# Optimization experiments

Hardware: AMD Instinct MI355X
Metric: run time of the kernel (lower is better)

The kernel has to match this reference:

```python
import jax, jax.numpy as jnp
import numpy as np

N_NODES = 100000
N_EDGES = 1600000
D_IN = 50
HIDDEN = 128
N_CLASSES = 8


def setup_inputs() -> dict:
    key = jax.random.key(0)
    ks = jax.random.split(key, 8)
    x = jax.random.normal(ks[0], (N_NODES, D_IN), dtype=jnp.float32)
    edge_index = jax.random.randint(ks[1], (2, N_EDGES), 0, N_NODES, dtype=jnp.int64)
    s1 = 1.0 / np.sqrt(D_IN)
    s2 = 1.0 / np.sqrt(HIDDEN)
    return {
        "x": x,
        "edge_index": edge_index,
        "W1_l": jax.random.normal(ks[2], (D_IN, HIDDEN), dtype=jnp.float32) * s1,
        "W1_r": jax.random.normal(ks[3], (D_IN, HIDDEN), dtype=jnp.float32) * s1,
        "b1": jnp.zeros((HIDDEN,), dtype=jnp.float32),
        "W2_l": jax.random.normal(ks[4], (HIDDEN, N_CLASSES), dtype=jnp.float32) * s2,
        "W2_r": jax.random.normal(ks[5], (HIDDEN, N_CLASSES), dtype=jnp.float32) * s2,
        "b2": jnp.zeros((N_CLASSES,), dtype=jnp.float32),
    }


def _sage_conv(h, src, dst, n_nodes, W_l, W_r, b):
    # mean aggregation of neighbor messages src -> dst
    msg = h[src]                                                   # [E, d]
    agg = jax.ops.segment_sum(msg, dst, num_segments=n_nodes)      # [N, d]
    deg = jax.ops.segment_sum(jnp.ones((src.shape[0], 1), h.dtype), dst,
                              num_segments=n_nodes)                # [N, 1]
    agg = agg / jnp.maximum(deg, 1.0)
    # PyG SAGEConv: lin_l(aggregated) + lin_r(root), bias in lin_l
    return agg @ W_l + h @ W_r + b


def reference(x, edge_index, W1_l, W1_r, b1, W2_l, W2_r, b2):
    n_nodes = x.shape[0]
    src, dst = edge_index[0], edge_index[1]
    h = jax.nn.relu(_sage_conv(x, src, dst, n_nodes, W1_l, W1_r, b1))
    # dropout p=0.5 is identity in eval mode (deterministic baseline)
    return _sage_conv(h, src, dst, n_nodes, W2_l, W2_r, b2)
```

## Files before the change

### kernel.cpp

```cpp
#include <hip/hip_runtime.h>

#define N_NODES 100000
#define N_EDGES 1600000
#define D_IN    50
#define HIDDEN  128
#define NCLS    8

#define TILE    4096
#define NTILES  ((N_EDGES + TILE - 1) / TILE)
#define BSHIFT  9
#define NB      196

#define PREP_CONVX_BLOCKS 12500
#define PREP_W_BLOCKS     36

#define LW 68

typedef __bf16 bf16_t;
typedef bf16_t bf16x8 __attribute__((ext_vector_type(8)));
typedef float  f32x4  __attribute__((ext_vector_type(4)));

__device__ __forceinline__ unsigned f2bf(float f) {
    union { float f; unsigned u; } a; a.f = f;
    unsigned u = a.u;
    return (u + 0x7FFFu + ((u >> 16) & 1u)) >> 16;
}
__device__ __forceinline__ unsigned pack2(float a, float b) {
    return f2bf(a) | (f2bf(b) << 16);
}
__device__ __forceinline__ float bf_lo(unsigned v) { return __uint_as_float(v << 16); }
__device__ __forceinline__ float bf_hi(unsigned v) { return __uint_as_float(v & 0xFFFF0000u); }

__global__ __launch_bounds__(256) void prep_kernel(
    const float* __restrict__ x,
    const int*   __restrict__ dst,
    const float* __restrict__ W1l, const float* __restrict__ W1r,
    const float* __restrict__ W2l, const float* __restrict__ W2r,
    unsigned* __restrict__ xb, unsigned* __restrict__ acat,
    int* __restrict__ g_hist, int* __restrict__ btot,
    unsigned* __restrict__ Wt1g, unsigned* __restrict__ W2tg)
{
    __shared__ int lh[NB];
    int blk = blockIdx.x;
    int tid = threadIdx.x;

    if (blk < PREP_CONVX_BLOCKS) {
        int t = blk * 256 + tid;
        int n = t >> 5, j = t & 31;
        if (j < 25) {
            float2 v = ((const float2*)x)[n * 25 + j];
            unsigned pk = pack2(v.x, v.y);
            xb[n * 25 + j] = pk;
            acat[(size_t)n * 64 + 25 + j] = pk;
        } else {
            int z = n * 64 + 50 + (j - 25) * 2;
            acat[z] = 0u;
            acat[z + 1] = 0u;
        }
    } else if (blk < PREP_CONVX_BLOCKS + NTILES) {
        int tile = blk - PREP_CONVX_BLOCKS;
        for (int i = tid; i < NB; i += 256) lh[i] = 0;
        __syncthreads();
        int base = tile * TILE;
        int cnt = min(TILE, N_EDGES - base);
        for (int i = tid; i < cnt; i += 256)
            atomicAdd(&lh[dst[base + i] >> BSHIFT], 1);
        __syncthreads();
        for (int i = tid; i < NB; i += 256) {
            int v = lh[i];
            g_hist[tile * NB + i] = v;
            if (v) atomicAdd(&btot[i], v);
        }
    } else {
        int t = (blk - PREP_CONVX_BLOCKS - NTILES) * 256 + tid;
        if (t < 8192) {
            int n = t >> 6, kp = t & 63;
            int k0 = kp * 2, k1 = k0 + 1;
            float v0 = (k0 < 50) ? W1l[k0 * 128 + n] : ((k0 < 100) ? W1r[(k0 - 50) * 128 + n] : 0.0f);
            float v1 = (k1 < 50) ? W1l[k1 * 128 + n] : ((k1 < 100) ? W1r[(k1 - 50) * 128 + n] : 0.0f);
            Wt1g[t] = pack2(v0, v1);
        } else if (t < 8192 + 1024) {
            int u = t - 8192;
            int n2 = u >> 6, kp = u & 63;
            int k0 = kp * 2;
            float v0 = (n2 < 8) ? W2l[k0 * 8 + n2] : W2r[k0 * 8 + n2 - 8];
            float v1 = (n2 < 8) ? W2l[(k0 + 1) * 8 + n2] : W2r[(k0 + 1) * 8 + n2 - 8];
            W2tg[u] = pack2(v0, v1);
        }
    }
}

__global__ __launch_bounds__(512) void passB_kernel(
    int* __restrict__ g_hist, const int* __restrict__ btot,
    int* __restrict__ bbase, int* __restrict__ offs)
{
    __shared__ int s[512];
    int b = blockIdx.x, tid = threadIdx.x;
    int v = (tid < NTILES) ? g_hist[tid * NB + b] : 0;
    s[tid] = v;
    __syncthreads();
    for (int d = 1; d < 512; d <<= 1) {
        int t = (tid >= d) ? s[tid - d] : 0;
        __syncthreads();
        s[tid] += t;
        __syncthreads();
    }
    if (tid < NTILES) g_hist[tid * NB + b] = s[tid] - v;
    __syncthreads();

    int v2 = (tid < NB) ? btot[tid] : 0;
    s[tid] = v2;
    __syncthreads();
    for (int d = 1; d < 256; d <<= 1) {
        int t = (tid >= d && tid < 256) ? s[tid - d] : 0;
        __syncthreads();
        if (tid < 256) s[tid] += t;
        __syncthreads();
    }
    if (tid == b) bbase[b] = s[tid] - v2;
    if (b == 0 && tid == 0) offs[N_NODES] = N_EDGES;
}

__global__ __launch_bounds__(256) void passC_kernel(
    const int* __restrict__ src, const int* __restrict__ dst,
    const int* __restrict__ g_hist, const int* __restrict__ bbase,
    unsigned* __restrict__ bk_pack)
{
    __shared__ int hist[NB];
    __shared__ int seg[NB];
    __shared__ int cur[NB];
    __shared__ int gof[NB];
    __shared__ int sc[256];
    __shared__ unsigned s_pack[TILE];
    __shared__ unsigned short s_bkt[TILE];

    int tid = threadIdx.x, tile = blockIdx.x;
    int base = tile * TILE;
    int cnt = min(TILE, N_EDGES - base);

    for (int i = tid; i < NB; i += 256) {
        hist[i] = 0;
        gof[i] = g_hist[tile * NB + i] + bbase[i];
    }
    __syncthreads();

    int es[16], ed[16];
    #pragma unroll
    for (int k = 0; k < 16; ++k) {
        int i = tid + k * 256;
        if (i < cnt) {
            es[k] = src[base + i];
            ed[k] = dst[base + i];
            atomicAdd(&hist[ed[k] >> BSHIFT], 1);
        }
    }
    __syncthreads();

    {
        int v = (tid < NB) ? hist[tid] : 0;
        sc[tid] = v;
        __syncthreads();
        for (int d = 1; d < 256; d <<= 1) {
            int t = (tid >= d) ? sc[tid - d] : 0;
            __syncthreads();
            sc[tid] += t;
            __syncthreads();
        }
        if (tid < NB) { seg[tid] = sc[tid] - v; cur[tid] = sc[tid] - v; }
    }
    __syncthreads();

    #pragma unroll
    for (int k = 0; k < 16; ++k) {
        int i = tid + k * 256;
        if (i < cnt) {
            int b = ed[k] >> BSHIFT;
            int p = atomicAdd(&cur[b], 1);
            s_pack[p] = (unsigned)es[k] | ((unsigned)(ed[k] & 511) << 17);
            s_bkt[p] = (unsigned short)b;
        }
    }
    __syncthreads();

    for (int i = tid; i < cnt; i += 256) {
        int b = s_bkt[i];
        int g = gof[b] + (i - seg[b]);
        bk_pack[g] = s_pack[i];
    }
}

__global__ __launch_bounds__(512) void passD_kernel(
    const unsigned* __restrict__ bk_pack,
    const int* __restrict__ bbase, const int* __restrict__ btot,
    int* __restrict__ sorted_src, int* __restrict__ offs)
{
    __shared__ int ldeg[512];
    __shared__ int lofs[512];
    int b = blockIdx.x, tid = threadIdx.x;
    int ebase = bbase[b];
    int ecnt = btot[b];
    int nbase = b << BSHIFT;

    ldeg[tid] = 0;
    __syncthreads();
    for (int i = tid; i < ecnt; i += 512)
        atomicAdd(&ldeg[bk_pack[ebase + i] >> 17], 1);
    __syncthreads();

    int v = ldeg[tid];
    lofs[tid] = v;
    __syncthreads();
    for (int d = 1; d < 512; d <<= 1) {
        int t = (tid >= d) ? lofs[tid - d] : 0;
        __syncthreads();
        lofs[tid] += t;
        __syncthreads();
    }
    int ex = lofs[tid] - v;

    int node = nbase + tid;
    if (node < N_NODES) offs[node] = ebase + ex;

    ldeg[tid] = ex;
    __syncthreads();
    for (int i = tid; i < ecnt; i += 512) {
        unsigned pk = bk_pack[ebase + i];
        int p = atomicAdd(&ldeg[pk >> 17], 1);
        sorted_src[ebase + p] = (int)(pk & 0x1FFFFu);
    }
}

__global__ __launch_bounds__(256) void agg_x_kernel(
    const unsigned* __restrict__ xb,
    const int*      __restrict__ offs,
    const int*      __restrict__ ss,
    unsigned* __restrict__ acat)
{
    int node = blockIdx.x * 8 + (threadIdx.x >> 5);
    int dw   = threadIdx.x & 31;
    if (node >= N_NODES) return;
    int beg = offs[node], end = offs[node + 1];
    float2 a0 = {0.f,0.f}, a1 = {0.f,0.f}, a2 = {0.f,0.f}, a3 = {0.f,0.f};
    float2 a4 = {0.f,0.f}, a5 = {0.f,0.f}, a6 = {0.f,0.f}, a7 = {0.f,0.f};
    int i = beg;
    for (; i + 7 < end; i += 8) {
        int s0 = ss[i],     s1 = ss[i + 1], s2 = ss[i + 2], s3 = ss[i + 3];
        int s4 = ss[i + 4], s5 = ss[i + 5], s6 = ss[i + 6], s7 = ss[i + 7];
        if (dw < 25) {
            unsigned v0 = xb[s0 * 25 + dw];
            unsigned v1 = xb[s1 * 25 + dw];
            unsigned v2 = xb[s2 * 25 + dw];
            unsigned v3 = xb[s3 * 25 + dw];
            unsigned v4 = xb[s4 * 25 + dw];
            unsigned v5 = xb[s5 * 25 + dw];
            unsigned v6 = xb[s6 * 25 + dw];
            unsigned v7 = xb[s7 * 25 + dw];
            a0.x += bf_lo(v0); a0.y += bf_hi(v0);
            a1.x += bf_lo(v1); a1.y += bf_hi(v1);
            a2.x += bf_lo(v2); a2.y += bf_hi(v2);
            a3.x += bf_lo(v3); a3.y += bf_hi(v3);
            a4.x += bf_lo(v4); a4.y += bf_hi(v4);
            a5.x += bf_lo(v5); a5.y += bf_hi(v5);
            a6.x += bf_lo(v6); a6.y += bf_hi(v6);
            a7.x += bf_lo(v7); a7.y += bf_hi(v7);
        }
    }
    for (; i + 3 < end; i += 4) {
        int s0 = ss[i], s1 = ss[i + 1], s2 = ss[i + 2], s3 = ss[i + 3];
        if (dw < 25) {
            unsigned v0 = xb[s0 * 25 + dw];
            unsigned v1 = xb[s1 * 25 + dw];
            unsigned v2 = xb[s2 * 25 + dw];
            unsigned v3 = xb[s3 * 25 + dw];
            a0.x += bf_lo(v0); a0.y += bf_hi(v0);
            a1.x += bf_lo(v1); a1.y += bf_hi(v1);
            a2.x += bf_lo(v2); a2.y += bf_hi(v2);
            a3.x += bf_lo(v3); a3.y += bf_hi(v3);
        }
    }
    for (; i < end; ++i) {
        int s = ss[i];
        if (dw < 25) {
            unsigned v = xb[s * 25 + dw];
            a0.x += bf_lo(v); a0.y += bf_hi(v);
        }
    }
    if (dw < 25) {
        float inv = 1.0f / fmaxf((float)(end - beg), 1.0f);
        float sx = ((a0.x + a1.x) + (a2.x + a3.x)) + ((a4.x + a5.x) + (a6.x + a7.x));
        float sy = ((a0.y + a1.y) + (a2.y + a3.y)) + ((a4.y + a5.y) + (a6.y + a7.y));
        acat[(size_t)node * 64 + dw] = pack2(sx * inv, sy * inv);
    }
}

__global__ __launch_bounds__(256) void fused_mlp_kernel(
    const unsigned* __restrict__ Acat,
    const unsigned* __restrict__ Wt1g,
    const unsigned* __restrict__ W2tg,
    const float* __restrict__ b1,
    const float* __restrict__ b2,
    unsigned* __restrict__ pb,
    float* __restrict__ q)
{
    __shared__ unsigned sWt[128 * LW];
    __shared__ unsigned sW2t[16 * LW];
    __shared__ bf16_t   sH[4][16 * 136];

    int tid = threadIdx.x;
    for (int t = tid; t < 128 * 64; t += 256)
        sWt[(t >> 6) * LW + (t & 63)] = Wt1g[t];
    for (int t = tid; t < 16 * 64; t += 256)
        sW2t[(t >> 6) * LW + (t & 63)] = W2tg[t];
    __syncthreads();

    const int w    = tid >> 6;
    const int lane = tid & 63;
    const int lo   = lane & 15;
    const int g    = lane >> 4;

    float b1v[8][4];
    #pragma unroll
    for (int nt = 0; nt < 8; ++nt)
        #pragma unroll
        for (int r = 0; r < 4; ++r)
            b1v[nt][r] = b1[nt * 16 + g * 4 + r];
    float b2v[4];
    #pragma unroll
    for (int r = 0; r < 4; ++r)
        b2v[r] = (g >= 2) ? b2[(g - 2) * 4 + r] : 0.0f;

    bf16_t* myH = &sH[w][0];

    for (int tile = blockIdx.x; tile * 64 < N_NODES; tile += gridDim.x) {
        int node = tile * 64 + w * 16 + lo;
        int nclamp = min(node, N_NODES - 1);

        int4 bi[4];
        #pragma unroll
        for (int ks = 0; ks < 4; ++ks)
            bi[ks] = *((const int4*)(Acat + (size_t)nclamp * 64 + ks * 16 + g * 4));

        f32x4 acc[8];
        #pragma unroll
        for (int nt = 0; nt < 8; ++nt) acc[nt] = (f32x4)0.0f;
        #pragma unroll
        for (int nt = 0; nt < 8; ++nt) {
            #pragma unroll
            for (int ks = 0; ks < 4; ++ks) {
                int4 ai = *((const int4*)(sWt + (nt * 16 + lo) * LW + ks * 16 + g * 4));
                acc[nt] = __builtin_amdgcn_mfma_f32_16x16x32_bf16(
                    __builtin_bit_cast(bf16x8, ai),
                    __builtin_bit_cast(bf16x8, bi[ks]), acc[nt], 0, 0, 0);
            }
        }

        #pragma unroll
        for (int nt = 0; nt < 8; ++nt) {
            union { bf16_t h[4]; uint2 u; } pk;
            #pragma unroll
            for (int r = 0; r < 4; ++r)
                pk.h[r] = (bf16_t)fmaxf(acc[nt][r] + b1v[nt][r], 0.0f);
            *((uint2*)(myH + lo * 136 + nt * 16 + g * 4)) = pk.u;
        }
        __syncthreads();

        f32x4 acc2 = (f32x4)0.0f;
        #pragma unroll
        for (int ks = 0; ks < 4; ++ks) {
            int4 a2 = *((const int4*)(sW2t + lo * LW + ks * 16 + g * 4));
            int4 h2 = *((const int4*)(myH + lo * 136 + ks * 32 + g * 8));
            acc2 = __builtin_amdgcn_mfma_f32_16x16x32_bf16(
                __builtin_bit_cast(bf16x8, a2),
                __builtin_bit_cast(bf16x8, h2), acc2, 0, 0, 0);
        }

        if (node < N_NODES) {
            if (g < 2) {
                union { bf16_t h[4]; uint2 u; } pk;
                #pragma unroll
                for (int r = 0; r < 4; ++r) pk.h[r] = (bf16_t)acc2[r];
                *((uint2*)(pb + (size_t)node * 4 + g * 2)) = pk.u;
            } else {
                float4 qq;
                qq.x = acc2[0] + b2v[0];
                qq.y = acc2[1] + b2v[1];
                qq.z = acc2[2] + b2v[2];
                qq.w = acc2[3] + b2v[3];
                *((float4*)(q + (size_t)node * 8 + (g - 2) * 4)) = qq;
            }
        }
        __syncthreads();
    }
}

__global__ __launch_bounds__(256) void aggp_final_kernel(
    const unsigned* __restrict__ pb,
    const float*    __restrict__ q,
    const int*      __restrict__ offs,
    const int*      __restrict__ ss,
    float* __restrict__ out)
{
    int node = blockIdx.x * 4 + (threadIdx.x >> 6);
    int lane = threadIdx.x & 63;
    int k  = lane >> 2;
    int c2 = lane & 3;
    if (node >= N_NODES) return;
    int beg = offs[node], end = offs[node + 1];
    float2 acc = make_float2(0.0f, 0.0f);
    int i = beg + k;
    int sNext = (i < end) ? ss[i] : 0;
    for (; i < end; i += 16) {
        int s = sNext;
        int i2 = i + 16;
        sNext = (i2 < end) ? ss[i2] : 0;
        unsigned v = pb[s * 4 + c2];
        acc.x += bf_lo(v);
        acc.y += bf_hi(v);
    }
    acc.x += __shfl_xor(acc.x, 4);  acc.y += __shfl_xor(acc.y, 4);
    acc.x += __shfl_xor(acc.x, 8);  acc.y += __shfl_xor(acc.y, 8);
    acc.x += __shfl_xor(acc.x, 16); acc.y += __shfl_xor(acc.y, 16);
    acc.x += __shfl_xor(acc.x, 32); acc.y += __shfl_xor(acc.y, 32);
    if (lane < 4) {
        float inv = 1.0f / fmaxf((float)(end - beg), 1.0f);
        float2 qq = ((const float2*)(q + (size_t)node * NCLS))[c2];
        ((float2*)(out + (size_t)node * NCLS))[c2] =
            make_float2(acc.x * inv + qq.x, acc.y * inv + qq.y);
    }
}

extern "C" void kernel_launch(void* const* d_in, const int* in_sizes, int n_in,
                              void* d_out, int out_size, void* d_ws, size_t ws_size,
                              hipStream_t stream)
{
    const float* x   = (const float*)d_in[0];
    const int*   ei  = (const int*)  d_in[1];
    const float* W1l = (const float*)d_in[2];
    const float* W1r = (const float*)d_in[3];
    const float* b1  = (const float*)d_in[4];
    const float* W2l = (const float*)d_in[5];
    const float* W2r = (const float*)d_in[6];
    const float* b2  = (const float*)d_in[7];
    float* out = (float*)d_out;

    const int* src = ei;
    const int* dst = ei + N_EDGES;

    int* ws = (int*)d_ws;
    int*      offs       = ws;
    int*      g_hist     = offs + (N_NODES + 4);
    int*      btot       = g_hist + NTILES * NB;
    int*      bbase      = btot + 256;
    int*      sorted_src = bbase + 256;
    unsigned* xb         = (unsigned*)(sorted_src + N_EDGES);
    unsigned* Acat       = xb + (size_t)N_NODES * 25;
    unsigned* Wt1g       = Acat + (size_t)N_NODES * 64;
    unsigned* W2tg       = Wt1g + 8192;
    unsigned* pb         = W2tg + 1024;
    float*    q          = (float*)(pb + (size_t)N_NODES * 4);
    unsigned* bk_pack    = (unsigned*)(q + (size_t)N_NODES * 8);

    (void)hipMemsetAsync(btot, 0, NB * sizeof(int), stream);

    prep_kernel<<<PREP_CONVX_BLOCKS + NTILES + PREP_W_BLOCKS, 256, 0, stream>>>(
        x, dst, W1l, W1r, W2l, W2r, xb, Acat, g_hist, btot, Wt1g, W2tg);

    passB_kernel<<<NB, 512, 0, stream>>>(g_hist, btot, bbase, offs);
    passC_kernel<<<NTILES, 256, 0, stream>>>(src, dst, g_hist, bbase, bk_pack);
    passD_kernel<<<NB, 512, 0, stream>>>(bk_pack, bbase, btot, sorted_src, offs);

    agg_x_kernel<<<(N_NODES + 7) / 8, 256, 0, stream>>>(xb, offs, sorted_src, Acat);

    fused_mlp_kernel<<<512, 256, 0, stream>>>(Acat, Wt1g, W2tg, b1, b2, pb, q);

    aggp_final_kernel<<<(N_NODES + 3) / 4, 256, 0, stream>>>(
        (const unsigned*)pb, q, offs, sorted_src, out);
}
```

Baseline: 140.3 us.

## Pad bf16 features to 32 words and gather neighbours with 16-byte vector loads

The bf16 copy of x is padded from 25 to 32 words per row so that the first-layer neighbour gather can use uint4 loads. In each half-wave, four neighbours are processed in parallel with eight lanes per row, and the partial sums are combined with xor shuffles. This replaces 32-bit loads where 7 of 32 lanes sat idle. The sort tile is also halved to 2048 edges so more blocks run, and passB now scans two tiles per thread to handle the larger tile count. The cost is more memory for the padded array and some shuffle overhead.

```diff
diff --git a/kernel.cpp b/kernel.cpp
--- a/kernel.cpp
+++ b/kernel.cpp
@@ -6,7 +6,7 @@
 #define HIDDEN  128
 #define NCLS    8
 
-#define TILE    4096
+#define TILE    2048
 #define NTILES  ((N_EDGES + TILE - 1) / TILE)
 #define BSHIFT  9
 #define NB      196
@@ -30,6 +30,9 @@
 }
 __device__ __forceinline__ float bf_lo(unsigned v) { return __uint_as_float(v << 16); }
 __device__ __forceinline__ float bf_hi(unsigned v) { return __uint_as_float(v & 0xFFFF0000u); }
+
+#define ACC4(a, u) { a[0]+=bf_lo(u.x); a[1]+=bf_hi(u.x); a[2]+=bf_lo(u.y); a[3]+=bf_hi(u.y); \
+                     a[4]+=bf_lo(u.z); a[5]+=bf_hi(u.z); a[6]+=bf_lo(u.w); a[7]+=bf_hi(u.w); }
 
 __global__ __launch_bounds__(256) void prep_kernel(
     const float* __restrict__ x,
@@ -50,9 +53,10 @@
         if (j < 25) {
             float2 v = ((const float2*)x)[n * 25 + j];
             unsigned pk = pack2(v.x, v.y);
-            xb[n * 25 + j] = pk;
+            xb[n * 32 + j] = pk;
             acat[(size_t)n * 64 + 25 + j] = pk;
         } else {
+            xb[n * 32 + j] = 0u;
             int z = n * 64 + 50 + (j - 25) * 2;
             acat[z] = 0u;
             acat[z + 1] = 0u;
@@ -96,7 +100,10 @@
 {
     __shared__ int s[512];
     int b = blockIdx.x, tid = threadIdx.x;
-    int v = (tid < NTILES) ? g_hist[tid * NB + b] : 0;
+    int t0 = 2 * tid, t1 = 2 * tid + 1;
+    int v0 = (t0 < NTILES) ? g_hist[t0 * NB + b] : 0;
+    int v1 = (t1 < NTILES) ? g_hist[t1 * NB + b] : 0;
+    int v = v0 + v1;
     s[tid] = v;
     __syncthreads();
     for (int d = 1; d < 512; d <<= 1) {
@@ -105,16 +112,18 @@
         s[tid] += t;
         __syncthreads();
     }
-    if (tid < NTILES) g_hist[tid * NB + b] = s[tid] - v;
+    int ex = s[tid] - v;
+    if (t0 < NTILES) g_hist[t0 * NB + b] = ex;
+    if (t1 < NTILES) g_hist[t1 * NB + b] = ex + v0;
     __syncthreads();
 
     int v2 = (tid < NB) ? btot[tid] : 0;
     s[tid] = v2;
     __syncthreads();
-    for (int d = 1; d < 256; d <<= 1) {
-        int t = (tid >= d && tid < 256) ? s[tid - d] : 0;
-        __syncthreads();
-        if (tid < 256) s[tid] += t;
+    for (int d = 1; d < 512; d <<= 1) {
+        int t = (tid >= d) ? s[tid - d] : 0;
+        __syncthreads();
+        s[tid] += t;
         __syncthreads();
     }
     if (tid == b) bbase[b] = s[tid] - v2;
@@ -144,9 +153,9 @@
     }
     __syncthreads();
 
-    int es[16], ed[16];
+    int es[8], ed[8];
     #pragma unroll
-    for (int k = 0; k < 16; ++k) {
+    for (int k = 0; k < 8; ++k) {
         int i = tid + k * 256;
         if (i < cnt) {
             es[k] = src[base + i];
@@ -171,7 +180,7 @@
     __syncthreads();
 
     #pragma unroll
-    for (int k = 0; k < 16; ++k) {
+    for (int k = 0; k < 8; ++k) {
         int i = tid + k * 256;
         if (i < cnt) {
             int b = ed[k] >> BSHIFT;
@@ -231,65 +240,57 @@
 }
 
 __global__ __launch_bounds__(256) void agg_x_kernel(
-    const unsigned* __restrict__ xb,
-    const int*      __restrict__ offs,
-    const int*      __restrict__ ss,
+    const uint4* __restrict__ xb4,
+    const int*   __restrict__ offs,
+    const int*   __restrict__ ss,
     unsigned* __restrict__ acat)
 {
     int node = blockIdx.x * 8 + (threadIdx.x >> 5);
-    int dw   = threadIdx.x & 31;
+    int l32  = threadIdx.x & 31;
+    int slot = l32 >> 3;
+    int ld   = l32 & 7;
     if (node >= N_NODES) return;
     int beg = offs[node], end = offs[node + 1];
-    float2 a0 = {0.f,0.f}, a1 = {0.f,0.f}, a2 = {0.f,0.f}, a3 = {0.f,0.f};
-    float2 a4 = {0.f,0.f}, a5 = {0.f,0.f}, a6 = {0.f,0.f}, a7 = {0.f,0.f};
+    float a0[8] = {0,0,0,0,0,0,0,0};
+    float a1[8] = {0,0,0,0,0,0,0,0};
     int i = beg;
     for (; i + 7 < end; i += 8) {
-        int s0 = ss[i],     s1 = ss[i + 1], s2 = ss[i + 2], s3 = ss[i + 3];
-        int s4 = ss[i + 4], s5 = ss[i + 5], s6 = ss[i + 6], s7 = ss[i + 7];
-        if (dw < 25) {
-            unsigned v0 = xb[s0 * 25 + dw];
-            unsigned v1 = xb[s1 * 25 + dw];
-            unsigned v2 = xb[s2 * 25 + dw];
-            unsigned v3 = xb[s3 * 25 + dw];
-            unsigned v4 = xb[s4 * 25 + dw];
-            unsigned v5 = xb[s5 * 25 + dw];
-            unsigned v6 = xb[s6 * 25 + dw];
-            unsigned v7 = xb[s7 * 25 + dw];
-            a0.x += bf_lo(v0); a0.y += bf_hi(v0);
-            a1.x += bf_lo(v1); a1.y += bf_hi(v1);
-            a2.x += bf_lo(v2); a2.y += bf_hi(v2);
-            a3.x += bf_lo(v3); a3.y += bf_hi(v3);
-            a4.x += bf_lo(v4); a4.y += bf_hi(v4);
-            a5.x += bf_lo(v5); a5.y += bf_hi(v5);
-            a6.x += bf_lo(v6); a6.y += bf_hi(v6);
-            a7.x += bf_lo(v7); a7.y += bf_hi(v7);
-        }
+        int s0 = ss[i + slot];
+        int s1 = ss[i + slot + 4];
+        uint4 u0 = xb4[s0 * 8 + ld];
+        uint4 u1 = xb4[s1 * 8 + ld];
+        ACC4(a0, u0);
+        ACC4(a1, u1);
     }
     for (; i + 3 < end; i += 4) {
-        int s0 = ss[i], s1 = ss[i + 1], s2 = ss[i + 2], s3 = ss[i + 3];
-        if (dw < 25) {
-            unsigned v0 = xb[s0 * 25 + dw];
-            unsigned v1 = xb[s1 * 25 + dw];
-            unsigned v2 = xb[s2 * 25 + dw];
-            unsigned v3 = xb[s3 * 25 + dw];
-            a0.x += bf_lo(v0); a0.y += bf_hi(v0);
-            a1.x += bf_lo(v1); a1.y += bf_hi(v1);
-            a2.x += bf_lo(v2); a2.y += bf_hi(v2);
-            a3.x += bf_lo(v3); a3.y += bf_hi(v3);
-        }
-    }
-    for (; i < end; ++i) {
-        int s = ss[i];
-        if (dw < 25) {
-            unsigned v = xb[s * 25 + dw];
-            a0.x += bf_lo(v); a0.y += bf_hi(v);
-        }
-    }
-    if (dw < 25) {
+        uint4 u = xb4[ss[i + slot] * 8 + ld];
+        ACC4(a0, u);
+    }
+    int rem = end - i;
+    if (slot < rem) {
+        uint4 u = xb4[ss[i + slot] * 8 + ld];
+        ACC4(a1, u);
+    }
+    float t[8];
+    #pragma unroll
+    for (int k = 0; k < 8; ++k) {
+        float v = a0[k] + a1[k];
+        v += __shfl_xor(v, 8);
+        v += __shfl_xor(v, 16);
+        t[k] = v;
+    }
+    if (slot == 0) {
         float inv = 1.0f / fmaxf((float)(end - beg), 1.0f);
-        float sx = ((a0.x + a1.x) + (a2.x + a3.x)) + ((a4.x + a5.x) + (a6.x + a7.x));
-        float sy = ((a0.y + a1.y) + (a2.y + a3.y)) + ((a4.y + a5.y) + (a6.y + a7.y));
-        acat[(size_t)node * 64 + dw] = pack2(sx * inv, sy * inv);
+        if (ld < 6) {
+            uint4 o;
+            o.x = pack2(t[0] * inv, t[1] * inv);
+            o.y = pack2(t[2] * inv, t[3] * inv);
+            o.z = pack2(t[4] * inv, t[5] * inv);
+            o.w = pack2(t[6] * inv, t[7] * inv);
+            *((uint4*)(acat + (size_t)node * 64 + ld * 4)) = o;
+        } else if (ld == 6) {
+            acat[(size_t)node * 64 + 24] = pack2(t[0] * inv, t[1] * inv);
+        }
     }
 }
 
@@ -449,11 +450,11 @@
     int* ws = (int*)d_ws;
     int*      offs       = ws;
     int*      g_hist     = offs + (N_NODES + 4);
-    int*      btot       = g_hist + NTILES * NB;
-    int*      bbase      = btot + 256;
-    int*      sorted_src = bbase + 256;
+    int*      btot       = g_hist + (NTILES * NB + 4);
+    int*      bbase      = btot + 512;
+    int*      sorted_src = bbase + 512;
     unsigned* xb         = (unsigned*)(sorted_src + N_EDGES);
-    unsigned* Acat       = xb + (size_t)N_NODES * 25;
+    unsigned* Acat       = xb + (size_t)N_NODES * 32;
     unsigned* Wt1g       = Acat + (size_t)N_NODES * 64;
     unsigned* W2tg       = Wt1g + 8192;
     unsigned* pb         = W2tg + 1024;
@@ -469,7 +470,8 @@
     passC_kernel<<<NTILES, 256, 0, stream>>>(src, dst, g_hist, bbase, bk_pack);
     passD_kernel<<<NB, 512, 0, stream>>>(bk_pack, bbase, btot, sorted_src, offs);
 
-    agg_x_kernel<<<(N_NODES + 7) / 8, 256, 0, stream>>>(xb, offs, sorted_src, Acat);
+    agg_x_kernel<<<(N_NODES + 7) / 8, 256, 0, stream>>>(
+        (const uint4*)xb, offs, sorted_src, Acat);
 
     fused_mlp_kernel<<<512, 256, 0, stream>>>(Acat, Wt1g, W2tg, b1, b2, pb, q);
 
```

Result: faster. 137.2 us (-2.2%).
